# Performance work log

Measured on AMD Instinct MI355X. Metric: run time of the kernel, lower is better.

The kernel has to match this reference:

```python
import jax, jax.numpy as jnp
import numpy as np

B, SX, TY = 256, 180, 160
D, DK, DV, H, DFF, V = 512, 64, 64, 8, 2048, 30
EPS = 1e-5


def _ln(x, g, b):
    m = jnp.mean(x, axis=-1, keepdims=True)
    v = jnp.mean(jnp.square(x - m), axis=-1, keepdims=True)
    return (x - m) / jnp.sqrt(v + EPS) * g + b


def _mha(q, kv, wq, wk, wv, pw, pb, masked):
    # per-head projections, vectorized over heads (source loops in Python)
    C = q.shape[-1]  # scale uses d_model (input dim), faithful to source
    Q = jnp.einsum('btd,hdk->bhtk', q, wq)
    K = jnp.einsum('bsd,hdk->bhsk', kv, wk)
    Vv = jnp.einsum('bsd,hdv->bhsv', kv, wv)
    W = jnp.einsum('bhtk,bhsk->bhts', Q, K) / (C ** 0.5)
    if masked:
        T = q.shape[1]
        tri = jnp.tril(jnp.ones((T, T), dtype=bool))
        W = jnp.where(tri, W, -jnp.inf)
    W = jax.nn.softmax(W, axis=-1)  # dropout is identity at rate 0 / eval
    out = jnp.einsum('bhts,bhsv->bthv', W, Vv)
    out = out.reshape(q.shape[0], q.shape[1], -1)  # concat heads -> [B,T,H*DV]
    return out @ pw + pb


def _attn_block(q, kv, wq, wk, wv, pw, pb, g, b, masked):
    res = q + _mha(q, kv, wq, wk, wv, pw, pb, masked)
    return _ln(res, g, b)


def _ff_block(x, w1, b1, w2, b2, g, b):
    h = jax.nn.relu(x @ w1 + b1) @ w2 + b2
    return _ln(x + h, g, b)


def setup_inputs() -> dict:
    key = jax.random.key(0)
    ks = iter(jax.random.split(key, 64))

    def n(shape, s=0.05):
        return jax.random.normal(next(ks), shape, jnp.float32) * s

    inp = {}
    inp['x'] = jax.random.normal(next(ks), (B, SX, 2), jnp.float32)
    inp['targets'] = jax.random.randint(next(ks), (B, TY + 1), 0, V, jnp.int32)
    inp['spec_w'] = n((2, D), 0.5)
    inp['spec_b'] = jnp.zeros((D,), jnp.float32)
    inp['pep_emb'] = n((V, D), 0.5)
    for p in ['enc_at', 'dec_sat', 'dec_cat']:
        inp[p + '_wq'] = n((H, D, DK))
        inp[p + '_wk'] = n((H, D, DK))
        inp[p + '_wv'] = n((H, D, DV))
        inp[p + '_pw'] = n((H * DV, D))
        inp[p + '_pb'] = jnp.zeros((D,), jnp.float32)
        inp[p + '_g'] = jnp.ones((D,), jnp.float32)
        inp[p + '_b'] = jnp.zeros((D,), jnp.float32)
    for p in ['enc_ff', 'dec_ff']:
        inp[p + '_w1'] = n((D, DFF))
        inp[p + '_b1'] = jnp.zeros((DFF,), jnp.float32)
        inp[p + '_w2'] = n((DFF, D))
        inp[p + '_b2'] = jnp.zeros((D,), jnp.float32)
        inp[p + '_g'] = jnp.ones((D,), jnp.float32)
        inp[p + '_b'] = jnp.zeros((D,), jnp.float32)
    inp['ll_w'] = n((D, V))
    inp['ll_b'] = jnp.zeros((V,), jnp.float32)
    return inp


def reference(x, targets, spec_w, spec_b, pep_emb,
              enc_at_wq, enc_at_wk, enc_at_wv, enc_at_pw, enc_at_pb, enc_at_g, enc_at_b,
              dec_sat_wq, dec_sat_wk, dec_sat_wv, dec_sat_pw, dec_sat_pb, dec_sat_g, dec_sat_b,
              dec_cat_wq, dec_cat_wk, dec_cat_wv, dec_cat_pw, dec_cat_pb, dec_cat_g, dec_cat_b,
              enc_ff_w1, enc_ff_b1, enc_ff_w2, enc_ff_b2, enc_ff_g, enc_ff_b,
              dec_ff_w1, dec_ff_b1, dec_ff_w2, dec_ff_b2, dec_ff_g, dec_ff_b,
              ll_w, ll_b):
    tgt = targets[:, :-1]
    xe = x @ spec_w + spec_b                      # spectrum embedding [B,SX,D]
    enc = _attn_block(xe, xe, enc_at_wq, enc_at_wk, enc_at_wv, enc_at_pw, enc_at_pb, enc_at_g, enc_at_b, False)
    enc = _ff_block(enc, enc_ff_w1, enc_ff_b1, enc_ff_w2, enc_ff_b2, enc_ff_g, enc_ff_b)
    de = pep_emb[tgt]                             # peptide embedding [B,TY,D]
    d1 = _attn_block(de, de, dec_sat_wq, dec_sat_wk, dec_sat_wv, dec_sat_pw, dec_sat_pb, dec_sat_g, dec_sat_b, True)
    d2 = _attn_block(d1, enc, dec_cat_wq, dec_cat_wk, dec_cat_wv, dec_cat_pw, dec_cat_pb, dec_cat_g, dec_cat_b, False)
    d3 = _ff_block(d2, dec_ff_w1, dec_ff_b1, dec_ff_w2, dec_ff_b2, dec_ff_g, dec_ff_b)
    return d3 @ ll_w + ll_b                       # logits [B,TY,V]
```

## Files before the change

kernel.cpp:

```cpp
#include <hip/hip_runtime.h>
#include <hip/hip_bf16.h>

typedef __hip_bfloat16 bf16;
typedef __attribute__((ext_vector_type(8))) short short8;
typedef __attribute__((ext_vector_type(4))) float f32x4;

#define BB   256
#define SXX  180
#define TYY  160
#define DD   512
#define DKK  64
#define HH   8
#define DFFF 2048
#define VV   30

#define NE (BB * SXX)
#define ND (BB * TYY)
#define N_IN 40

#ifndef __has_builtin
#define __has_builtin(x) 0
#endif

__global__ void k_detect(const unsigned short* __restrict__ probe, int* __restrict__ flag)
{
    if (threadIdx.x == 0 && blockIdx.x == 0)
        *flag = (probe[0] != 0x3F80) ? 1 : 0;
}

__device__ __forceinline__ float ldin(const void* src, long i, int f32)
{
    return f32 ? ((const float*)src)[i] : __bfloat162float(((const bf16*)src)[i]);
}

struct ImpD { const void* src; bf16* dst; int n; int K; int N; int mode; int blk0; int pad; };
struct ImpT { ImpD d[N_IN]; };

__global__ __launch_bounds__(256) void k_import_all(ImpT t, const int* __restrict__ flag)
{
    const int bid = blockIdx.x;
    int which = 0;
    #pragma unroll
    for (int k = 1; k < N_IN; ++k)
        if (bid >= t.d[k].blk0) which = k;
    ImpD d = t.d[which];
    if (d.mode == 3) return;
    long li = (long)(bid - d.blk0) * 256 + threadIdx.x;
    if (li >= d.n) return;
    int f32 = *flag;
    float v;
    if (d.mode == 0) {
        v = ldin(d.src, li, f32);
    } else if (d.mode == 1) {
        int nrow = (int)(li / d.K);
        int k    = (int)(li - (long)nrow * d.K);
        v = (nrow < d.N) ? ldin(d.src, (long)k * d.N + nrow, f32) : 0.f;
    } else {
        int n1 = (int)(li >> 9), dd = (int)(li & 511);
        v = ldin(d.src, (long)(n1 >> 6) * (DD * DKK) + (long)dd * DKK + (n1 & 63), f32);
    }
    d.dst[li] = __float2bfloat16(v);
}

__global__ __launch_bounds__(256) void k_embed_spec(
    const bf16* __restrict__ x, const bf16* __restrict__ w,
    const bf16* __restrict__ b, bf16* __restrict__ out)
{
    long i = (long)blockIdx.x * 256 + threadIdx.x;
    if (i >= (long)NE * DD) return;
    long tok = i >> 9;
    int  d   = (int)(i & 511);
    float x0 = __bfloat162float(x[tok * 2 + 0]);
    float x1 = __bfloat162float(x[tok * 2 + 1]);
    out[i] = __float2bfloat16(x0 * __bfloat162float(w[d])
                            + x1 * __bfloat162float(w[DD + d])
                            + __bfloat162float(b[d]));
}

__global__ __launch_bounds__(256) void k_gather(
    const int* __restrict__ tg, const bf16* __restrict__ emb, bf16* __restrict__ out)
{
    long tok = blockIdx.x;
    int  b   = (int)(tok / TYY);
    int  t   = (int)(tok - (long)b * TYY);
    int  idx = tg[(long)b * (TYY + 1) + t];
    const bf16* src = emb + (long)idx * DD;
    bf16*       dst = out + tok * DD;
    dst[threadIdx.x]       = src[threadIdx.x];
    dst[threadIdx.x + 256] = src[threadIdx.x + 256];
}

__device__ __forceinline__ void stage16(const bf16* g, bf16* l)
{
#if __has_builtin(__builtin_amdgcn_global_load_lds)
    __builtin_amdgcn_global_load_lds(
        (const __attribute__((address_space(1))) unsigned int*)g,
        (__attribute__((address_space(3))) unsigned int*)l, 16, 0, 0);
#else
    *(short8*)l = *(const short8*)g;
#endif
}

__global__ __launch_bounds__(256, 1) void k_mgemm(
    const bf16* __restrict__ A, const bf16* __restrict__ BT,
    const bf16* __restrict__ bias, const bf16* __restrict__ res,
    void* __restrict__ C,
    int M, int N, int K, int lda, int ldb, int ldc,
    int relu, const int* __restrict__ outf32)
{
    __shared__ __align__(16) bf16 sh[16384];

    const int tid  = threadIdx.x;
    const int lane = tid & 63;
    const int w    = tid >> 6;
    const int m0   = blockIdx.y * 128;
    const int n0   = blockIdx.x * 128;
    const int mw   = (w >> 1) * 64;
    const int nw   = (w & 1) * 64;

    f32x4 acc[4][4];
    #pragma unroll
    for (int i = 0; i < 4; ++i)
        #pragma unroll
        for (int j = 0; j < 4; ++j)
            acc[i][j] = (f32x4){0.f, 0.f, 0.f, 0.f};

    const int  sr = tid >> 2;
    const int  kq = ((tid & 3) - ((sr >> 1) & 3)) & 3;
    const int  sk = kq * 8;
    const bf16* Ag0 = A  + (size_t)(m0 + sr) * lda + sk;
    const bf16* Ag1 = Ag0 + (size_t)64 * lda;
    const bf16* Bg0 = BT + (size_t)(n0 + sr) * ldb + sk;
    const bf16* Bg1 = Bg0 + (size_t)64 * ldb;
    const int lofs = tid * 8;

    const int lc = lane & 15, lq = lane >> 4;
    const int sl = (lq + ((lc >> 1) & 3)) & 3;

    stage16(Ag0, sh + lofs);
    stage16(Ag1, sh + 2048 + lofs);
    stage16(Bg0, sh + 4096 + lofs);
    stage16(Bg1, sh + 6144 + lofs);

    for (int k0 = 0; k0 < K; k0 += 32) {
        bf16* cb = sh + ((k0 >> 5) & 1) * 8192;
        __syncthreads();
        if (k0 + 32 < K) {
            bf16* nb = sh + ((~(k0 >> 5)) & 1) * 8192;
            stage16(Ag0 + k0 + 32, nb + lofs);
            stage16(Ag1 + k0 + 32, nb + 2048 + lofs);
            stage16(Bg0 + k0 + 32, nb + 4096 + lofs);
            stage16(Bg1 + k0 + 32, nb + 6144 + lofs);
        }

        short8 af[4], bfr[4];
        #pragma unroll
        for (int i = 0; i < 4; ++i)
            af[i] = *(const short8*)(cb + (mw + i * 16 + lc) * 32 + sl * 8);
        #pragma unroll
        for (int j = 0; j < 4; ++j)
            bfr[j] = *(const short8*)(cb + 4096 + (nw + j * 16 + lc) * 32 + sl * 8);

        #pragma unroll
        for (int i = 0; i < 4; ++i)
            #pragma unroll
            for (int j = 0; j < 4; ++j)
                acc[i][j] = __builtin_amdgcn_mfma_f32_16x16x32_bf16(
                    af[i], bfr[j], acc[i][j], 0, 0, 0);
    }

    const int f32o = (outf32 != nullptr) ? *outf32 : 0;

    if (!f32o && (N & 127) == 0) {
        float bv[4];
        #pragma unroll
        for (int j = 0; j < 4; ++j)
            bv[j] = bias ? __bfloat162float(bias[n0 + nw + j * 16 + lc]) : 0.f;
        bf16* ep = sh;
        #pragma unroll
        for (int i = 0; i < 4; ++i) {
            __syncthreads();
            #pragma unroll
            for (int j = 0; j < 4; ++j)
                #pragma unroll
                for (int r = 0; r < 4; ++r) {
                    float v = acc[i][j][r] + bv[j];
                    if (relu && v < 0.f) v = 0.f;
                    int lr = (w >> 1) * 16 + lq * 4 + r;
                    ep[lr * 136 + nw + j * 16 + lc] = __float2bfloat16(v);
                }
            __syncthreads();
            #pragma unroll
            for (int u = 0; u < 2; ++u) {
                int slot = tid + 256 * u;
                int lr   = slot >> 4;
                int cb2  = (slot & 15) << 3;
                int gm   = m0 + 16 * i + ((lr & 16) ? (48 + lr) : lr);
                int gn   = n0 + cb2;
                short8 val = *(short8*)(ep + lr * 136 + cb2);
                if (res) {
                    short8 rv = *(const short8*)(res + (size_t)gm * ldc + gn);
                    #pragma unroll
                    for (int e = 0; e < 8; ++e) {
                        float s = __bfloat162float(((bf16*)&val)[e])
                                + __bfloat162float(((bf16*)&rv)[e]);
                        ((bf16*)&val)[e] = __float2bfloat16(s);
                    }
                }
                *(short8*)((bf16*)C + (size_t)gm * ldc + gn) = val;
            }
        }
    } else {
        #pragma unroll
        for (int j = 0; j < 4; ++j) {
            int gn = n0 + nw + j * 16 + lc;
            if (gn >= N) continue;
            float bvj = bias ? __bfloat162float(bias[gn]) : 0.f;
            #pragma unroll
            for (int i = 0; i < 4; ++i) {
                int gm = m0 + mw + i * 16 + lq * 4;
                #pragma unroll
                for (int r = 0; r < 4; ++r) {
                    float v = acc[i][j][r] + bvj;
                    if (relu && v < 0.f) v = 0.f;
                    size_t off = (size_t)(gm + r) * ldc + gn;
                    if (res) v += __bfloat162float(res[off]);
                    if (f32o) ((float*)C)[off] = v;
                    else      ((bf16*)C)[off]  = __float2bfloat16(v);
                }
            }
        }
    }
}

__global__ __launch_bounds__(256, 1) void k_fattn(
    const bf16* __restrict__ Q, const bf16* __restrict__ Kc,
    const bf16* __restrict__ Vt, bf16* __restrict__ O,
    int T, int S, int b_off, int causal, int ldv)
{
    __shared__ __align__(16) bf16 Pl[4 * 48 * 72];
    const int bl = blockIdx.x, h = blockIdx.y;
    const int tid = threadIdx.x, lane = tid & 63, w = tid >> 6;
    const int lc = lane & 15, lq = lane >> 4;
    const int wr0 = w * 48;
    const float scl = 0.044194173824159216f;

    short8 Qf[3][2];
    #pragma unroll
    for (int i = 0; i < 3; ++i) {
        int t = wr0 + 16 * i + lc;
        if (t >= T) t = T - 1;
        const bf16* qp = Q + ((size_t)(bl + b_off) * T + t) * DD + h * 64;
        #pragma unroll
        for (int kt = 0; kt < 2; ++kt)
            Qf[i][kt] = *(const short8*)(qp + kt * 32 + lq * 8);
    }

    float mrow[3][4], lrow[3][4];
    f32x4 oacc[3][4];
    #pragma unroll
    for (int i = 0; i < 3; ++i)
        #pragma unroll
        for (int r = 0; r < 4; ++r) { mrow[i][r] = -1e30f; lrow[i][r] = 0.f; }
    #pragma unroll
    for (int i = 0; i < 3; ++i)
        #pragma unroll
        for (int n = 0; n < 4; ++n)
            oacc[i][n] = (f32x4){0.f, 0.f, 0.f, 0.f};

    bf16* pw = Pl + w * 48 * 72;

    for (int c0 = 0; c0 < 192; c0 += 64) {
        if (causal && c0 > wr0 + 47) continue;

        short8 Kf[4][2];
        #pragma unroll
        for (int j = 0; j < 4; ++j) {
            int s = c0 + 16 * j + lc;
            if (s >= S) s = S - 1;
            const bf16* kp = Kc + ((size_t)bl * S + s) * DD + h * 64;
            #pragma unroll
            for (int kt = 0; kt < 2; ++kt)
                Kf[j][kt] = *(const short8*)(kp + kt * 32 + lq * 8);
        }

        f32x4 sa[3][4];
        #pragma unroll
        for (int i = 0; i < 3; ++i)
            #pragma unroll
            for (int j = 0; j < 4; ++j)
                sa[i][j] = (f32x4){0.f, 0.f, 0.f, 0.f};
        #pragma unroll
        for (int i = 0; i < 3; ++i)
            #pragma unroll
            for (int j = 0; j < 4; ++j)
                #pragma unroll
                for (int kt = 0; kt < 2; ++kt)
                    sa[i][j] = __builtin_amdgcn_mfma_f32_16x16x32_bf16(
                        Qf[i][kt], Kf[j][kt], sa[i][j], 0, 0, 0);

        #pragma unroll
        for (int i = 0; i < 3; ++i)
            #pragma unroll
            for (int j = 0; j < 4; ++j) {
                int col = c0 + 16 * j + lc;
                #pragma unroll
                for (int r = 0; r < 4; ++r) {
                    int row = wr0 + 16 * i + lq * 4 + r;
                    float v = sa[i][j][r] * scl;
                    if (col >= S || (causal && col > row)) v = -1e30f;
                    sa[i][j][r] = v;
                }
            }

        float corr[3][4];
        #pragma unroll
        for (int i = 0; i < 3; ++i)
            #pragma unroll
            for (int r = 0; r < 4; ++r) {
                float cm = fmaxf(fmaxf(sa[i][0][r], sa[i][1][r]),
                                 fmaxf(sa[i][2][r], sa[i][3][r]));
                cm = fmaxf(cm, __shfl_xor(cm, 1));
                cm = fmaxf(cm, __shfl_xor(cm, 2));
                cm = fmaxf(cm, __shfl_xor(cm, 4));
                cm = fmaxf(cm, __shfl_xor(cm, 8));
                float mn = fmaxf(mrow[i][r], cm);
                corr[i][r] = __expf(mrow[i][r] - mn);
                mrow[i][r] = mn;
            }
        #pragma unroll
        for (int i = 0; i < 3; ++i)
            #pragma unroll
            for (int j = 0; j < 4; ++j)
                #pragma unroll
                for (int r = 0; r < 4; ++r)
                    sa[i][j][r] = __expf(sa[i][j][r] - mrow[i][r]);
        #pragma unroll
        for (int i = 0; i < 3; ++i)
            #pragma unroll
            for (int r = 0; r < 4; ++r) {
                float sm = sa[i][0][r] + sa[i][1][r] + sa[i][2][r] + sa[i][3][r];
                sm += __shfl_xor(sm, 1);
                sm += __shfl_xor(sm, 2);
                sm += __shfl_xor(sm, 4);
                sm += __shfl_xor(sm, 8);
                lrow[i][r] = lrow[i][r] * corr[i][r] + sm;
            }

        #pragma unroll
        for (int i = 0; i < 3; ++i)
            #pragma unroll
            for (int j = 0; j < 4; ++j)
                #pragma unroll
                for (int r = 0; r < 4; ++r)
                    pw[(16 * i + lq * 4 + r) * 72 + 16 * j + lc] =
                        __float2bfloat16(sa[i][j][r]);

        short8 Pf[3][2], Vf[4][2];
        #pragma unroll
        for (int i = 0; i < 3; ++i)
            #pragma unroll
            for (int kt = 0; kt < 2; ++kt)
                Pf[i][kt] = *(const short8*)(pw + (16 * i + lc) * 72 + kt * 32 + lq * 8);
        #pragma unroll
        for (int n = 0; n < 4; ++n)
            #pragma unroll
            for (int kt = 0; kt < 2; ++kt)
                Vf[n][kt] = *(const short8*)(Vt + (size_t)(h * 64 + 16 * n + lc) * ldv
                                             + (size_t)bl * S + c0 + kt * 32 + lq * 8);

        #pragma unroll
        for (int i = 0; i < 3; ++i)
            #pragma unroll
            for (int n = 0; n < 4; ++n) {
                #pragma unroll
                for (int r = 0; r < 4; ++r)
                    oacc[i][n][r] *= corr[i][r];
                #pragma unroll
                for (int kt = 0; kt < 2; ++kt)
                    oacc[i][n] = __builtin_amdgcn_mfma_f32_16x16x32_bf16(
                        Pf[i][kt], Vf[n][kt], oacc[i][n], 0, 0, 0);
            }
    }

    #pragma unroll
    for (int i = 0; i < 3; ++i)
        #pragma unroll
        for (int r = 0; r < 4; ++r) {
            int t = wr0 + 16 * i + lq * 4 + r;
            if (t >= T) continue;
            float inv = 1.f / lrow[i][r];
            bf16* op = O + ((size_t)(bl + b_off) * T + t) * DD + h * 64;
            #pragma unroll
            for (int n = 0; n < 4; ++n)
                op[16 * n + lc] = __float2bfloat16(oacc[i][n][r] * inv);
        }
}

__global__ __launch_bounds__(256) void k_ln(
    const bf16* __restrict__ in, const bf16* __restrict__ g,
    const bf16* __restrict__ b, bf16* __restrict__ out)
{
    __shared__ float red[256];
    long long base = (long long)blockIdx.x * DD;
    int tid = threadIdx.x;
    float v0 = __bfloat162float(in[base + tid]);
    float v1 = __bfloat162float(in[base + 256 + tid]);

    red[tid] = v0 + v1; __syncthreads();
    for (int st = 128; st > 0; st >>= 1) {
        if (tid < st) red[tid] += red[tid + st];
        __syncthreads();
    }
    float mean = red[0] * (1.f / DD);
    __syncthreads();

    float d0 = v0 - mean, d1 = v1 - mean;
    red[tid] = d0 * d0 + d1 * d1; __syncthreads();
    for (int st = 128; st > 0; st >>= 1) {
        if (tid < st) red[tid] += red[tid + st];
        __syncthreads();
    }
    float rstd = rsqrtf(red[0] * (1.f / DD) + 1e-5f);

    out[base + tid] = __float2bfloat16(d0 * rstd * __bfloat162float(g[tid])
                                       + __bfloat162float(b[tid]));
    out[base + 256 + tid] = __float2bfloat16(d1 * rstd * __bfloat162float(g[tid + 256])
                                             + __bfloat162float(b[tid + 256]));
}

static inline void mgemm(hipStream_t s, const bf16* A, const bf16* BT, const bf16* bias,
                         const bf16* res, void* C, int M, int N, int K,
                         int lda, int ldb, int ldc, int relu, const int* outf32 = nullptr)
{
    dim3 grid((N + 127) / 128, M / 128);
    k_mgemm<<<grid, dim3(256), 0, s>>>(A, BT, bias, res, C, M, N, K, lda, ldb, ldc,
                                       relu, outf32);
}

extern "C" void kernel_launch(void* const* d_in, const int* in_sizes, int n_in,
                              void* d_out, int out_size, void* d_ws, size_t ws_size,
                              hipStream_t stream)
{
    char* base = (char*)d_ws;
    size_t o = 0;
    auto take = [&](size_t bytes) { size_t r = o; o += (bytes + 255) & ~(size_t)255; return r; };

    int* dflag = (int*)(base + take(256));
    k_detect<<<dim3(1), dim3(64), 0, stream>>>((const unsigned short*)d_in[10], dflag);

    ImpT tab;
    int blk = 0;
    const bf16* cv[N_IN];
    auto add_imp = [&](int i, int mode, int K, int N, int n_elems) {
        bf16* dst = (bf16*)(base + take((size_t)n_elems * 2));
        tab.d[i] = ImpD{d_in[i], dst, n_elems, K, N, mode, blk, 0};
        blk += (n_elems + 255) / 256;
        cv[i] = dst;
    };
    for (int i = 0; i < N_IN; ++i) {
        if (i == 1) { tab.d[i] = ImpD{nullptr, nullptr, 0, 0, 0, 3, blk, 0}; cv[i] = nullptr; continue; }
        bool qkv = (i == 5 || i == 6 || i == 7 || i == 12 || i == 13 || i == 14 ||
                    i == 19 || i == 20 || i == 21);
        if (qkv)                        add_imp(i, 2, 0, 0, DD * DD);
        else if (i == 8 || i == 15 || i == 22) add_imp(i, 1, DD, DD, DD * DD);
        else if (i == 26 || i == 32)    add_imp(i, 1, DD, DFFF, DFFF * DD);
        else if (i == 28 || i == 34)    add_imp(i, 1, DFFF, DD, DD * DFFF);
        else if (i == 38)               add_imp(i, 1, DD, VV, 128 * DD);
        else                            add_imp(i, 0, 0, 0, in_sizes[i]);
    }
    k_import_all<<<dim3(blk), dim3(256), 0, stream>>>(tab, dflag);

    const int* targets = (const int*)d_in[1];
    const bf16 *x = cv[0], *spec_w = cv[2], *spec_b = cv[3], *pep_emb = cv[4];
    const bf16 *eat_wq = cv[5],  *eat_wk = cv[6],  *eat_wvT = cv[7],  *eat_pw = cv[8],
               *eat_pb = cv[9],  *eat_g  = cv[10], *eat_b   = cv[11];
    const bf16 *sat_wq = cv[12], *sat_wk = cv[13], *sat_wvT = cv[14], *sat_pw = cv[15],
               *sat_pb = cv[16], *sat_g  = cv[17], *sat_b   = cv[18];
    const bf16 *cat_wq = cv[19], *cat_wk = cv[20], *cat_wvT = cv[21], *cat_pw = cv[22],
               *cat_pb = cv[23], *cat_g  = cv[24], *cat_b   = cv[25];
    const bf16 *eff_w1 = cv[26], *eff_b1 = cv[27], *eff_w2 = cv[28], *eff_b2 = cv[29],
               *eff_g  = cv[30], *eff_b  = cv[31];
    const bf16 *dff_w1 = cv[32], *dff_b1 = cv[33], *dff_w2 = cv[34], *dff_b2 = cv[35],
               *dff_g  = cv[36], *dff_b  = cv[37];
    const bf16 *ll_w = cv[38], *ll_b = cv[39];

    const size_t REG = (size_t)NE * DD * 2;
    bf16* A = (bf16*)(base + take(REG));
    bf16* B = (bf16*)(base + take(REG));
    bf16* C = (bf16*)(base + take(REG));
    bf16* D = (bf16*)(base + take(REG + 4096));
    bf16* D2  = D + (size_t)(NE / 2) * DD;
    bf16* H   = B;

    k_embed_spec<<<dim3((NE * DD + 255) / 256), dim3(256), 0, stream>>>(x, spec_w, spec_b, A);

    mgemm(stream, A, eat_wq, nullptr, nullptr, B, NE, DD, DD, DD, DD, DD, 0);
    for (int hb = 0; hb < 2; ++hb) {
        const bf16* kv = A + (size_t)hb * (NE / 2) * DD;
        mgemm(stream, kv, eat_wk, nullptr, nullptr, D, NE / 2, DD, DD, DD, DD, DD, 0);
        mgemm(stream, eat_wvT, kv, nullptr, nullptr, D2, DD, NE / 2, DD, DD, DD, NE / 2, 0);
        k_fattn<<<dim3(BB / 2, HH), dim3(256), 0, stream>>>(
            B, D, D2, B, SXX, SXX, hb * (BB / 2), 0, NE / 2);
    }
    mgemm(stream, B, eat_pw, eat_pb, A, C, NE, DD, DD, DD, DD, DD, 0);
    k_ln<<<dim3(NE), dim3(256), 0, stream>>>(C, eat_g, eat_b, A);

    {
        const int CH = NE / 2;
        for (int c = 0; c < 2; ++c) {
            const bf16* Ain = A + (size_t)c * CH * DD;
            mgemm(stream, Ain, eff_w1, eff_b1, nullptr, H, CH, DFFF, DD, DD, DD, DFFF, 1);
            mgemm(stream, H, eff_w2, eff_b2, Ain, D + (size_t)c * CH * DD,
                  CH, DD, DFFF, DFFF, DFFF, DD, 0);
        }
        k_ln<<<dim3(NE), dim3(256), 0, stream>>>(D, eff_g, eff_b, D);
    }

    k_gather<<<dim3(ND), dim3(256), 0, stream>>>(targets, pep_emb, A);

    bf16* C2d = C + (size_t)(ND / 2) * DD;
    mgemm(stream, A, sat_wq, nullptr, nullptr, B, ND, DD, DD, DD, DD, DD, 0);
    for (int hb = 0; hb < 2; ++hb) {
        const bf16* kv = A + (size_t)hb * (ND / 2) * DD;
        mgemm(stream, kv, sat_wk, nullptr, nullptr, C, ND / 2, DD, DD, DD, DD, DD, 0);
        mgemm(stream, sat_wvT, kv, nullptr, nullptr, C2d, DD, ND / 2, DD, DD, DD, ND / 2, 0);
        k_fattn<<<dim3(BB / 2, HH), dim3(256), 0, stream>>>(
            B, C, C2d, B, TYY, TYY, hb * (BB / 2), 1, ND / 2);
    }
    mgemm(stream, B, sat_pw, sat_pb, A, C, ND, DD, DD, DD, DD, DD, 0);
    k_ln<<<dim3(ND), dim3(256), 0, stream>>>(C, sat_g, sat_b, A);

    bf16* C2e = C + (size_t)(NE / 2) * DD;
    mgemm(stream, A, cat_wq, nullptr, nullptr, B, ND, DD, DD, DD, DD, DD, 0);
    for (int hb = 0; hb < 2; ++hb) {
        const bf16* kv = D + (size_t)hb * (NE / 2) * DD;
        mgemm(stream, kv, cat_wk, nullptr, nullptr, C, NE / 2, DD, DD, DD, DD, DD, 0);
        mgemm(stream, cat_wvT, kv, nullptr, nullptr, C2e, DD, NE / 2, DD, DD, DD, NE / 2, 0);
        k_fattn<<<dim3(BB / 2, HH), dim3(256), 0, stream>>>(
            B, C, C2e, B, TYY, SXX, hb * (BB / 2), 0, NE / 2);
    }
    mgemm(stream, B, cat_pw, cat_pb, A, C, ND, DD, DD, DD, DD, DD, 0);
    k_ln<<<dim3(ND), dim3(256), 0, stream>>>(C, cat_g, cat_b, A);

    {
        const int CH = ND / 2;
        for (int c = 0; c < 2; ++c) {
            const bf16* Ain = A + (size_t)c * CH * DD;
            mgemm(stream, Ain, dff_w1, dff_b1, nullptr, H, CH, DFFF, DD, DD, DD, DFFF, 1);
            mgemm(stream, H, dff_w2, dff_b2, Ain, D + (size_t)c * CH * DD,
                  CH, DD, DFFF, DFFF, DFFF, DD, 0);
        }
        k_ln<<<dim3(ND), dim3(256), 0, stream>>>(D, dff_g, dff_b, D);
    }

    mgemm(stream, D, ll_w, ll_b, nullptr, d_out, ND, VV, DD, DD, DD, VV, 0, dflag);

    (void)in_sizes; (void)n_in; (void)out_size; (void)ws_size;
}
```

Before: 1.767 ms.

## Triple-buffer GEMM LDS staging with explicit vmcnt waits and prefetch distance two

Moves the bf16 MFMA GEMM from double to triple buffering in LDS. Tiles are prefetched two k-steps ahead with global_load_lds, and s_waitcnt vmcnt plus s_barrier replace __syncthreads. The aim is to hide global load latency behind more MFMA work. In exchange each block uses more LDS, the loop takes two barriers per iteration, and the hand-written wait counts rely on stage16 issuing exactly four loads per stage and on K being at least 64.

```diff
diff --git a/kernel.cpp b/kernel.cpp
--- a/kernel.cpp
+++ b/kernel.cpp
@@ -108,7 +108,7 @@
     int M, int N, int K, int lda, int ldb, int ldc,
     int relu, const int* __restrict__ outf32)
 {
-    __shared__ __align__(16) bf16 sh[16384];
+    __shared__ __align__(16) bf16 sh[24576];
 
     const int tid  = threadIdx.x;
     const int lane = tid & 63;
@@ -137,21 +137,29 @@
     const int lc = lane & 15, lq = lane >> 4;
     const int sl = (lq + ((lc >> 1) & 3)) & 3;
 
-    stage16(Ag0, sh + lofs);
-    stage16(Ag1, sh + 2048 + lofs);
-    stage16(Bg0, sh + 4096 + lofs);
-    stage16(Bg1, sh + 6144 + lofs);
-
-    for (int k0 = 0; k0 < K; k0 += 32) {
-        bf16* cb = sh + ((k0 >> 5) & 1) * 8192;
-        __syncthreads();
-        if (k0 + 32 < K) {
-            bf16* nb = sh + ((~(k0 >> 5)) & 1) * 8192;
-            stage16(Ag0 + k0 + 32, nb + lofs);
-            stage16(Ag1 + k0 + 32, nb + 2048 + lofs);
-            stage16(Bg0 + k0 + 32, nb + 4096 + lofs);
-            stage16(Bg1 + k0 + 32, nb + 6144 + lofs);
-        }
+    const int kiters = K >> 5;
+
+    {
+        bf16* b0 = sh;
+        stage16(Ag0, b0 + lofs);
+        stage16(Ag1, b0 + 2048 + lofs);
+        stage16(Bg0, b0 + 4096 + lofs);
+        stage16(Bg1, b0 + 6144 + lofs);
+        bf16* b1 = sh + 8192;
+        stage16(Ag0 + 32, b1 + lofs);
+        stage16(Ag1 + 32, b1 + 2048 + lofs);
+        stage16(Bg0 + 32, b1 + 4096 + lofs);
+        stage16(Bg1 + 32, b1 + 6144 + lofs);
+    }
+
+    for (int t = 0; t < kiters; ++t) {
+        bf16* cb = sh + (t % 3) * 8192;
+
+        if (t + 1 < kiters)
+            asm volatile("s_waitcnt vmcnt(4)" ::: "memory");
+        else
+            asm volatile("s_waitcnt vmcnt(0)" ::: "memory");
+        asm volatile("s_barrier" ::: "memory");
 
         short8 af[4], bfr[4];
         #pragma unroll
@@ -160,6 +168,18 @@
         #pragma unroll
         for (int j = 0; j < 4; ++j)
             bfr[j] = *(const short8*)(cb + 4096 + (nw + j * 16 + lc) * 32 + sl * 8);
+
+        asm volatile("s_waitcnt lgkmcnt(0)" ::: "memory");
+        asm volatile("s_barrier" ::: "memory");
+
+        if (t + 2 < kiters) {
+            bf16* nb = sh + ((t + 2) % 3) * 8192;
+            const int ko = (t + 2) * 32;
+            stage16(Ag0 + ko, nb + lofs);
+            stage16(Ag1 + ko, nb + 2048 + lofs);
+            stage16(Bg0 + ko, nb + 4096 + lofs);
+            stage16(Bg1 + ko, nb + 6144 + lofs);
+        }
 
         #pragma unroll
         for (int i = 0; i < 4; ++i)
```

Result: no change. 1.743 ms (-1.3%).
